# Kernel optimization log

Measured on AMD Instinct MI355X. Metric: run time of the kernel, lower is better.

## Reference

```python
import jax, jax.numpy as jnp
import numpy as np

N = 100_000      # num nodes
E = 100_000      # num hyperedges
NNZ = 1_600_000  # incidence entries (avg degree 16)
DIN = 128
DOUT = 128


def setup_inputs() -> dict:
    key = jax.random.key(0)
    k1, k2, k3, k4 = jax.random.split(key, 4)
    x = jax.random.normal(k1, (N, DIN), dtype=jnp.float32)
    weight = jax.random.normal(k2, (DIN, DOUT), dtype=jnp.float32) / np.sqrt(DIN).astype(np.float32)
    bias = jax.random.normal(k3, (DOUT,), dtype=jnp.float32) * 0.02
    hyperedge_index = jax.random.randint(k4, (2, NNZ), 0, N, dtype=jnp.int64)
    return {"x": x, "weight": weight, "bias": bias, "hyperedge_index": hyperedge_index}


def reference(x, weight, bias, hyperedge_index):
    # PyG HypergraphConv (use_attention=False, heads=1):
    #   out = D^{-1} H W B^{-1} H^T (x @ Theta) + bias, W = I (unit hyperedge weights)
    node_idx = hyperedge_index[0]  # [NNZ]
    edge_idx = hyperedge_index[1]  # [NNZ]

    h = x @ weight  # [N, DOUT]

    ones = jnp.ones((NNZ,), dtype=h.dtype)
    # node degree D_i = sum of hyperedge weights (=1) over incident hyperedges
    D = jax.ops.segment_sum(ones, node_idx, num_segments=N)   # [N]
    # hyperedge degree B_e = number of incident nodes
    B = jax.ops.segment_sum(ones, edge_idx, num_segments=E)   # [E]
    Dinv = jnp.where(D > 0, 1.0 / D, 0.0)
    Binv = jnp.where(B > 0, 1.0 / B, 0.0)

    # nodes -> hyperedges: m_e = B_e^{-1} * sum_{i in e} h_i
    e_feat = jax.ops.segment_sum(h[node_idx], edge_idx, num_segments=E) * Binv[:, None]  # [E, DOUT]
    # hyperedges -> nodes: out_i = D_i^{-1} * sum_{e ni i} m_e
    out = jax.ops.segment_sum(e_feat[edge_idx], node_idx, num_segments=N) * Dinv[:, None]  # [N, DOUT]
    return out + bias
```

## Files before the change

### kernel.cpp

```cpp
#include <hip/hip_runtime.h>

#define Nn 100000
#define Ne 100000
#define NNZC 1600000
#define NBLK 256
#define CHUNK 6250
#define BSH 8
#define NBK 391
#define CAPB 5120
#define GEMM_TOTAL 1563
#define NSUB 8
#define SUBW 32
#define QCAP 1024
#define NSG 3136

typedef __attribute__((ext_vector_type(8))) short short8;
typedef __attribute__((ext_vector_type(4))) float floatx4;

__device__ inline unsigned short f2bf(float f) {
    union { float f; unsigned int i; } c; c.f = f;
    unsigned int i = c.i;
    return (unsigned short)((i + 0x7fffu + ((i >> 16) & 1u)) >> 16);
}
__device__ inline unsigned int f2bf2(float lo, float hi) {
    union { float f; unsigned int i; } a, b;
    a.f = lo; b.f = hi;
    const unsigned int x = (a.i + 0x7fffu + ((a.i >> 16) & 1u)) >> 16;
    const unsigned int y = (b.i + 0x7fffu + ((b.i >> 16) & 1u)) & 0xffff0000u;
    return x | y;
}

union FusedLds {
    unsigned short wlds[128 * 136];
    struct { int a[NBK]; int b[NBK]; } s;
};

__device__ inline void gemm_block(int gb, const float* __restrict__ x,
                                  const float* __restrict__ w,
                                  unsigned short* __restrict__ h,
                                  unsigned short* wlds, int tid) {
    const int wave = tid >> 6, lane = tid & 63;
    const int q = lane >> 4, r16 = lane & 15;

    for (int i = tid; i < 4096; i += 256) {
        const int k = i >> 5;
        const int n0 = (i & 31) << 2;
        const float4 wv = *(const float4*)(w + k * 128 + n0);
        wlds[(n0 + 0) * 136 + k] = f2bf(wv.x);
        wlds[(n0 + 1) * 136 + k] = f2bf(wv.y);
        wlds[(n0 + 2) * 136 + k] = f2bf(wv.z);
        wlds[(n0 + 3) * 136 + k] = f2bf(wv.w);
    }
    __syncthreads();

    const int row0 = gb * 64 + wave * 16;
    const int rrow = min(row0 + r16, Nn - 1);

    floatx4 acc[8];
#pragma unroll
    for (int jb = 0; jb < 8; ++jb) acc[jb] = (floatx4){0.f, 0.f, 0.f, 0.f};

    const float* ap = x + (size_t)rrow * 128 + q * 8;
#pragma unroll
    for (int kk = 0; kk < 4; ++kk) {
        const float4 a0 = *(const float4*)(ap + kk * 32);
        const float4 a1 = *(const float4*)(ap + kk * 32 + 4);
        union { unsigned int u[4]; short8 s; } xf;
        xf.u[0] = f2bf2(a0.x, a0.y);
        xf.u[1] = f2bf2(a0.z, a0.w);
        xf.u[2] = f2bf2(a1.x, a1.y);
        xf.u[3] = f2bf2(a1.z, a1.w);
        const unsigned short* wp = wlds + kk * 32 + q * 8;
#pragma unroll
        for (int jb = 0; jb < 8; ++jb) {
            const short8 wf = *(const short8*)(wp + (jb * 16 + r16) * 136);
            acc[jb] = __builtin_amdgcn_mfma_f32_16x16x32_bf16(wf, xf.s, acc[jb], 0, 0, 0);
        }
    }

    if (row0 + r16 < Nn) {
        unsigned short* hb = h + (size_t)(row0 + r16) * 128 + q * 4;
#pragma unroll
        for (int jb = 0; jb < 8; ++jb) {
            uint2 o;
            o.x = f2bf2(acc[jb][0], acc[jb][1]);
            o.y = f2bf2(acc[jb][2], acc[jb][3]);
            *(uint2*)(hb + jb * 16) = o;
        }
    }
}

__global__ __launch_bounds__(256) void scatter_gemm_kernel(
        const int* __restrict__ nidx, const int* __restrict__ eidx,
        int* __restrict__ gcurN, int* __restrict__ gcurE,
        unsigned int* __restrict__ pairsN, unsigned int* __restrict__ pairsE,
        const float* __restrict__ x, const float* __restrict__ w,
        unsigned short* __restrict__ h) {
    __shared__ FusedLds sm;
    const int tid = threadIdx.x;
    if (blockIdx.x < NBLK) {
        for (int j = tid; j < NBK; j += 256) { sm.s.a[j] = 0; sm.s.b[j] = 0; }
        __syncthreads();
        const int base = blockIdx.x * CHUNK;
        for (int i = base + tid; i < base + CHUNK; i += 256) {
            atomicAdd(&sm.s.a[nidx[i] >> BSH], 1);
            atomicAdd(&sm.s.b[eidx[i] >> BSH], 1);
        }
        __syncthreads();
        for (int j = tid; j < NBK; j += 256) {
            sm.s.a[j] = atomicAdd(&gcurN[j], sm.s.a[j]);
            sm.s.b[j] = atomicAdd(&gcurE[j], sm.s.b[j]);
        }
        __syncthreads();
        for (int i = base + tid; i < base + CHUNK; i += 256) {
            const int n = nidx[i], e = eidx[i];
            const int pn = atomicAdd(&sm.s.a[n >> BSH], 1);
            if (pn < CAPB)
                pairsN[(size_t)(n >> BSH) * CAPB + pn] =
                    ((unsigned int)e << 8) | (unsigned int)(n & 255);
            const int pe = atomicAdd(&sm.s.b[e >> BSH], 1);
            if (pe < CAPB)
                pairsE[(size_t)(e >> BSH) * CAPB + pe] =
                    ((unsigned int)n << 8) | (unsigned int)(e & 255);
        }
    } else {
        gemm_block(blockIdx.x - NBLK, x, w, h, sm.wlds, tid);
    }
}

template <int MODE>
__global__ __launch_bounds__(256) void sortgather_kernel(
        const unsigned int* __restrict__ pairs, const int* __restrict__ gcur,
        const void* __restrict__ srcv, const float* __restrict__ bias,
        void* __restrict__ outv) {
    __shared__ int perm_lds[QCAP];
    __shared__ int offs_lds[SUBW + 1];
    __shared__ int cnt[SUBW];
    __shared__ int cur[SUBW];
    const int q0 = blockIdx.x;
    const int xs = q0 & 7, r = q0 >> 3;
    const int sub = r / 49;
    const int b = xs + ((r % 49) << 3);
    if (b >= NBK) return;
    const int tid = threadIdx.x;
    const int wave = tid >> 6, lane = tid & 63;

    if (tid < SUBW) cnt[tid] = 0;
    __syncthreads();

    const int fill = min(gcur[b], CAPB);
    const unsigned int* pb = pairs + (size_t)b * CAPB;

    for (int i = tid; i < fill; i += 256) {
        const unsigned int p = pb[i];
        if (((p >> 5) & 7u) == (unsigned int)sub)
            atomicAdd(&cnt[p & 31u], 1);
    }
    __syncthreads();
    if (tid == 0) {
        int s = 0;
        for (int i = 0; i < SUBW; ++i) {
            offs_lds[i] = s;
            cur[i] = s;
            s = min(s + cnt[i], QCAP);
        }
        offs_lds[SUBW] = s;
    }
    __syncthreads();
    for (int i = tid; i < fill; i += 256) {
        const unsigned int p = pb[i];
        if (((p >> 5) & 7u) == (unsigned int)sub) {
            const int pos = atomicAdd(&cur[p & 31u], 1);
            if (pos < QCAP) perm_lds[pos] = (int)(p >> 8);
        }
    }
    __syncthreads();

    const int i0 = wave << 3;
    const int start = offs_lds[i0];
    const int end = offs_lds[i0 + 8];
    const int pmax = offs_lds[SUBW] - 1;
    const unsigned int l4 = (unsigned int)lane << 2;
    const char* src = (const char*)srcv;

    float bx = 0.f, by = 0.f;
    if (MODE == 1) {
        const float2 bb = ((const float2*)bias)[lane];
        bx = bb.x; by = bb.y;
    }

    float ax = 0.f, ay = 0.f;
    int e = i0;
    int seg_start = start;
    int nb = offs_lds[i0 + 1];
    const int gidbase = (b << 8) + (sub << 5);

    auto flush = [&](int deg) {
        const int gid = gidbase + e;
        if (gid < 100000) {
            const float sinv = deg ? 1.f / (float)deg : 0.f;
            if (MODE == 0) {
                *(unsigned int*)((char*)outv + (((size_t)gid) << 8) + l4) =
                    f2bf2(ax * sinv, ay * sinv);
            } else {
                float2 o;
                o.x = ax * sinv + bx;
                o.y = ay * sinv + by;
                *(float2*)((char*)outv + (((size_t)gid) << 9) + ((size_t)l4 << 1)) = o;
            }
        }
        ax = 0.f; ay = 0.f;
        ++e;
    };

    int myv = 0;
    for (int i = start; i < end; i += 8) {
        const int t = (i - start) & 63;
        if (t == 0) myv = perm_lds[min(i + lane, pmax)];
        const int m = min(end - i, 8);
        unsigned int a[8], u[8];
#pragma unroll
        for (int j = 0; j < 8; ++j)
            a[j] = ((unsigned int)__shfl(myv, t + (j < m ? j : m - 1), 64) << 8) | l4;
#pragma unroll
        for (int j = 0; j < 8; ++j) u[j] = *(const unsigned int*)(src + a[j]);
#pragma unroll
        for (int j = 0; j < 8; ++j) {
            if (j < m) {
                while (i + j == nb) {
                    flush(nb - seg_start);
                    seg_start = nb;
                    nb = offs_lds[e + 1];
                }
                ax += __uint_as_float(u[j] << 16);
                ay += __uint_as_float(u[j] & 0xffff0000u);
            }
        }
    }
    while (e < i0 + 8) {
        flush(end - seg_start);
        seg_start = end;
    }
}

extern "C" void kernel_launch(void* const* d_in, const int* in_sizes, int n_in,
                              void* d_out, int out_size, void* d_ws, size_t ws_size,
                              hipStream_t stream) {
    const float* x = (const float*)d_in[0];
    const float* w = (const float*)d_in[1];
    const float* bias = (const float*)d_in[2];
    const int* hei = (const int*)d_in[3];
    const int* nidx = hei;
    const int* eidx = hei + NNZC;
    float* out = (float*)d_out;

    char* p = (char*)d_ws;
    unsigned short* h = (unsigned short*)p;  p += (size_t)Nn * 128 * 2;
    unsigned short* ef = (unsigned short*)p; p += (size_t)Ne * 128 * 2;
    int* gcurN = (int*)p;                    p += NBK * 4 + 192;
    int* gcurE = (int*)p;                    p += NBK * 4 + 192;
    unsigned int* pairsN = (unsigned int*)p; p += (size_t)NBK * CAPB * 4;
    unsigned int* pairsE = (unsigned int*)p; p += (size_t)NBK * CAPB * 4;

    hipMemsetAsync(gcurN, 0, 2 * (NBK * 4 + 192), stream);

    scatter_gemm_kernel<<<NBLK + GEMM_TOTAL, 256, 0, stream>>>(nidx, eidx, gcurN, gcurE,
                                                               pairsN, pairsE, x, w, h);
    sortgather_kernel<0><<<NSG, 256, 0, stream>>>(pairsE, gcurE, h, nullptr, ef);
    sortgather_kernel<1><<<NSG, 256, 0, stream>>>(pairsN, gcurN, ef, bias, out);
}
```

Before: 317.3 us.

## Split gather buckets in halves and process 256 GEMM rows per block

Each gather block now handles half of a 256-segment bucket (128 segments, 32 per wave) instead of one eighth, so each bucket's pair list is scanned twice instead of eight times. A parallel LDS prefix scan replaces the serial single-thread offset computation. The GEMM blocks now loop over 4 row groups of 64 rows, so the bf16 weight tile is staged into LDS once per 256 rows. The trade-off is fewer blocks with more serial work each, which can leave the GPU underoccupied and lower gather parallelism. It also needs larger LDS buffers with a higher capacity cap.

```diff
diff --git a/kernel.cpp b/kernel.cpp
--- a/kernel.cpp
+++ b/kernel.cpp
@@ -8,11 +8,9 @@
 #define BSH 8
 #define NBK 391
 #define CAPB 5120
-#define GEMM_TOTAL 1563
-#define NSUB 8
-#define SUBW 32
-#define QCAP 1024
-#define NSG 3136
+#define GEMM_TOTAL 391
+#define LCAP 2816
+#define NHB 782
 
 typedef __attribute__((ext_vector_type(8))) short short8;
 typedef __attribute__((ext_vector_type(4))) float floatx4;
@@ -35,10 +33,10 @@
     struct { int a[NBK]; int b[NBK]; } s;
 };
 
-__device__ inline void gemm_block(int gb, const float* __restrict__ x,
-                                  const float* __restrict__ w,
-                                  unsigned short* __restrict__ h,
-                                  unsigned short* wlds, int tid) {
+__device__ inline void gemm_block256(int gb, const float* __restrict__ x,
+                                     const float* __restrict__ w,
+                                     unsigned short* __restrict__ h,
+                                     unsigned short* wlds, int tid) {
     const int wave = tid >> 6, lane = tid & 63;
     const int q = lane >> 4, r16 = lane & 15;
 
@@ -53,39 +51,42 @@
     }
     __syncthreads();
 
-    const int row0 = gb * 64 + wave * 16;
-    const int rrow = min(row0 + r16, Nn - 1);
-
-    floatx4 acc[8];
-#pragma unroll
-    for (int jb = 0; jb < 8; ++jb) acc[jb] = (floatx4){0.f, 0.f, 0.f, 0.f};
-
-    const float* ap = x + (size_t)rrow * 128 + q * 8;
-#pragma unroll
-    for (int kk = 0; kk < 4; ++kk) {
-        const float4 a0 = *(const float4*)(ap + kk * 32);
-        const float4 a1 = *(const float4*)(ap + kk * 32 + 4);
-        union { unsigned int u[4]; short8 s; } xf;
-        xf.u[0] = f2bf2(a0.x, a0.y);
-        xf.u[1] = f2bf2(a0.z, a0.w);
-        xf.u[2] = f2bf2(a1.x, a1.y);
-        xf.u[3] = f2bf2(a1.z, a1.w);
-        const unsigned short* wp = wlds + kk * 32 + q * 8;
-#pragma unroll
-        for (int jb = 0; jb < 8; ++jb) {
-            const short8 wf = *(const short8*)(wp + (jb * 16 + r16) * 136);
-            acc[jb] = __builtin_amdgcn_mfma_f32_16x16x32_bf16(wf, xf.s, acc[jb], 0, 0, 0);
-        }
-    }
-
-    if (row0 + r16 < Nn) {
-        unsigned short* hb = h + (size_t)(row0 + r16) * 128 + q * 4;
-#pragma unroll
-        for (int jb = 0; jb < 8; ++jb) {
-            uint2 o;
-            o.x = f2bf2(acc[jb][0], acc[jb][1]);
-            o.y = f2bf2(acc[jb][2], acc[jb][3]);
-            *(uint2*)(hb + jb * 16) = o;
+#pragma unroll 1
+    for (int rg = 0; rg < 4; ++rg) {
+        const int row0 = gb * 256 + rg * 64 + wave * 16;
+        const int rrow = min(row0 + r16, Nn - 1);
+
+        floatx4 acc[8];
+#pragma unroll
+        for (int jb = 0; jb < 8; ++jb) acc[jb] = (floatx4){0.f, 0.f, 0.f, 0.f};
+
+        const float* ap = x + (size_t)rrow * 128 + q * 8;
+#pragma unroll
+        for (int kk = 0; kk < 4; ++kk) {
+            const float4 a0 = *(const float4*)(ap + kk * 32);
+            const float4 a1 = *(const float4*)(ap + kk * 32 + 4);
+            union { unsigned int u[4]; short8 s; } xf;
+            xf.u[0] = f2bf2(a0.x, a0.y);
+            xf.u[1] = f2bf2(a0.z, a0.w);
+            xf.u[2] = f2bf2(a1.x, a1.y);
+            xf.u[3] = f2bf2(a1.z, a1.w);
+            const unsigned short* wp = wlds + kk * 32 + q * 8;
+#pragma unroll
+            for (int jb = 0; jb < 8; ++jb) {
+                const short8 wf = *(const short8*)(wp + (jb * 16 + r16) * 136);
+                acc[jb] = __builtin_amdgcn_mfma_f32_16x16x32_bf16(wf, xf.s, acc[jb], 0, 0, 0);
+            }
+        }
+
+        if (row0 + r16 < Nn) {
+            unsigned short* hb = h + (size_t)(row0 + r16) * 128 + q * 4;
+#pragma unroll
+            for (int jb = 0; jb < 8; ++jb) {
+                uint2 o;
+                o.x = f2bf2(acc[jb][0], acc[jb][1]);
+                o.y = f2bf2(acc[jb][2], acc[jb][3]);
+                *(uint2*)(hb + jb * 16) = o;
+            }
         }
     }
 }
@@ -124,62 +125,67 @@
                     ((unsigned int)n << 8) | (unsigned int)(e & 255);
         }
     } else {
-        gemm_block(blockIdx.x - NBLK, x, w, h, sm.wlds, tid);
+        gemm_block256(blockIdx.x - NBLK, x, w, h, sm.wlds, tid);
     }
 }
 
 template <int MODE>
-__global__ __launch_bounds__(256) void sortgather_kernel(
+__global__ __launch_bounds__(256) void bucketgather_kernel(
         const unsigned int* __restrict__ pairs, const int* __restrict__ gcur,
         const void* __restrict__ srcv, const float* __restrict__ bias,
         void* __restrict__ outv) {
-    __shared__ int perm_lds[QCAP];
-    __shared__ int offs_lds[SUBW + 1];
-    __shared__ int cnt[SUBW];
-    __shared__ int cur[SUBW];
-    const int q0 = blockIdx.x;
-    const int xs = q0 & 7, r = q0 >> 3;
-    const int sub = r / 49;
-    const int b = xs + ((r % 49) << 3);
-    if (b >= NBK) return;
+    __shared__ int perm_lds[LCAP];
+    __shared__ int offs_lds[129];
+    __shared__ int cnt[128];
+    __shared__ int cur[128];
+    __shared__ int tmp[2][128];
+    const int b = blockIdx.x >> 1;
+    const int half = blockIdx.x & 1;
     const int tid = threadIdx.x;
     const int wave = tid >> 6, lane = tid & 63;
 
-    if (tid < SUBW) cnt[tid] = 0;
-    __syncthreads();
-
     const int fill = min(gcur[b], CAPB);
     const unsigned int* pb = pairs + (size_t)b * CAPB;
 
+    if (tid < 128) cnt[tid] = 0;
+    __syncthreads();
     for (int i = tid; i < fill; i += 256) {
         const unsigned int p = pb[i];
-        if (((p >> 5) & 7u) == (unsigned int)sub)
-            atomicAdd(&cnt[p & 31u], 1);
-    }
-    __syncthreads();
-    if (tid == 0) {
-        int s = 0;
-        for (int i = 0; i < SUBW; ++i) {
-            offs_lds[i] = s;
-            cur[i] = s;
-            s = min(s + cnt[i], QCAP);
-        }
-        offs_lds[SUBW] = s;
+        if ((int)((p >> 7) & 1u) == half) atomicAdd(&cnt[p & 127u], 1);
+    }
+    __syncthreads();
+    int v = 0, pin = 0;
+    if (tid < 128) { v = cnt[tid]; tmp[0][tid] = v; }
+    for (int off = 1; off < 128; off <<= 1) {
+        __syncthreads();
+        if (tid < 128) {
+            int val = tmp[pin][tid];
+            if (tid >= off) val += tmp[pin][tid - off];
+            tmp[1 - pin][tid] = val;
+        }
+        pin ^= 1;
+    }
+    __syncthreads();
+    if (tid < 128) {
+        const int excl = tmp[pin][tid] - v;
+        offs_lds[tid] = excl;
+        cur[tid] = excl;
+        if (tid == 127) offs_lds[128] = tmp[pin][127];
     }
     __syncthreads();
     for (int i = tid; i < fill; i += 256) {
         const unsigned int p = pb[i];
-        if (((p >> 5) & 7u) == (unsigned int)sub) {
-            const int pos = atomicAdd(&cur[p & 31u], 1);
-            if (pos < QCAP) perm_lds[pos] = (int)(p >> 8);
-        }
-    }
-    __syncthreads();
-
-    const int i0 = wave << 3;
+        if ((int)((p >> 7) & 1u) == half) {
+            const int pos = atomicAdd(&cur[p & 127u], 1);
+            if (pos < LCAP) perm_lds[pos] = (int)(p >> 8);
+        }
+    }
+    __syncthreads();
+
+    const int i0 = wave << 5;
     const int start = offs_lds[i0];
-    const int end = offs_lds[i0 + 8];
-    const int pmax = offs_lds[SUBW] - 1;
+    const int end = offs_lds[i0 + 32];
+    const int pmax = min(offs_lds[128], LCAP) - 1;
     const unsigned int l4 = (unsigned int)lane << 2;
     const char* src = (const char*)srcv;
 
@@ -193,7 +199,7 @@
     int e = i0;
     int seg_start = start;
     int nb = offs_lds[i0 + 1];
-    const int gidbase = (b << 8) + (sub << 5);
+    const int gidbase = (b << 8) + (half << 7);
 
     auto flush = [&](int deg) {
         const int gid = gidbase + e;
@@ -237,7 +243,7 @@
             }
         }
     }
-    while (e < i0 + 8) {
+    while (e < i0 + 32) {
         flush(end - seg_start);
         seg_start = end;
     }
@@ -266,6 +272,6 @@
 
     scatter_gemm_kernel<<<NBLK + GEMM_TOTAL, 256, 0, stream>>>(nidx, eidx, gcurN, gcurE,
                                                                pairsN, pairsE, x, w, h);
-    sortgather_kernel<0><<<NSG, 256, 0, stream>>>(pairsE, gcurE, h, nullptr, ef);
-    sortgather_kernel<1><<<NSG, 256, 0, stream>>>(pairsN, gcurN, ef, bias, out);
-}
+    bucketgather_kernel<0><<<NHB, 256, 0, stream>>>(pairsE, gcurE, h, nullptr, ef);
+    bucketgather_kernel<1><<<NHB, 256, 0, stream>>>(pairsN, gcurN, ef, bias, out);
+}
```

Measured after the change: 346.9 us. +9.3%, slower.
